# Optimization experiments

Hardware: AMD Instinct MI355X
Metric: run time of the kernel (lower is better)

## Reference

```python
import jax, jax.numpy as jnp
import numpy as np

N_ATOMS = 50000
N_EDGES = 1600000
N_ATOM_BASIS = 128
N_FILTERS = 128
N_BASIS = 25
CUTOFF = 5.0

def swish(x):
    return x * jax.nn.sigmoid(x)

def setup_inputs() -> dict:
    key = jax.random.key(0)
    ks = jax.random.split(key, 12)
    feat = jax.random.normal(ks[0], (N_ATOMS, N_ATOM_BASIS), dtype=jnp.float32)
    fij = jax.random.uniform(ks[1], (N_EDGES, N_BASIS), dtype=jnp.float32)  # RBF features in [0,1)
    rij = jax.random.uniform(ks[2], (N_EDGES,), dtype=jnp.float32) * CUTOFF  # distances in [0, cutoff)
    src = jax.random.randint(ks[3], (N_EDGES,), 0, N_ATOMS, dtype=jnp.int64)
    dst = jax.random.randint(ks[4], (N_EDGES,), 0, N_ATOMS, dtype=jnp.int64)
    s = 0.1
    W_in2f = jax.random.normal(ks[5], (N_ATOM_BASIS, N_FILTERS), dtype=jnp.float32) * s
    W_f1 = jax.random.normal(ks[6], (N_BASIS, N_FILTERS), dtype=jnp.float32) * s
    b_f1 = jax.random.normal(ks[7], (N_FILTERS,), dtype=jnp.float32) * s
    W_f2 = jax.random.normal(ks[8], (N_FILTERS, N_FILTERS), dtype=jnp.float32) * s
    b_f2 = jax.random.normal(ks[9], (N_FILTERS,), dtype=jnp.float32) * s
    W_out = jax.random.normal(ks[10], (N_FILTERS, N_ATOM_BASIS), dtype=jnp.float32) * s
    b_out = jax.random.normal(ks[11], (N_ATOM_BASIS,), dtype=jnp.float32) * s
    return {"feat": feat, "fij": fij, "rij": rij, "src": src, "dst": dst,
            "W_in2f": W_in2f, "W_f1": W_f1, "b_f1": b_f1,
            "W_f2": W_f2, "b_f2": b_f2, "W_out": W_out, "b_out": b_out}

def reference(feat, fij, rij, src, dst, W_in2f, W_f1, b_f1, W_f2, b_f2, W_out, b_out):
    # in2f: project node features to filter space (no bias, schnetpack CFConv)
    x = feat @ W_in2f                                            # [N, F]
    # filter network on RBF-expanded distances: Dense(swish) -> Dense
    Wfilt = swish(fij @ W_f1 + b_f1) @ W_f2 + b_f2               # [E, F]
    # cosine cutoff weighting
    C = 0.5 * (jnp.cos(rij * (jnp.pi / CUTOFF)) + 1.0)
    C = C * (rij < CUTOFF).astype(feat.dtype)                    # [E]
    # gather neighbor features, multiply by filter, scatter-sum to dst nodes
    m_edge = x[src] * Wfilt * C[:, None]                         # [E, F]
    agg = jax.ops.segment_sum(m_edge, dst, num_segments=N_ATOMS)  # [N, F]
    # f2out: project back to atom basis with swish activation
    return swish(agg @ W_out + b_out)                            # [N, n_atom_basis]
```

## Files before the change

### kernel.cpp

```cpp
#include <hip/hip_runtime.h>
#include <hip/hip_bf16.h>
#include <math.h>

#define N_ATOMS 50000
#define N_EDGES 1600000
#define FDIM 128
#define NB 25
#define CUTOFF_F 5.0f
#define PI_OVER_CUTOFF 0.6283185307179586f
#define NBLK 512
#define RB 196
#define P1B 782

typedef __bf16 bf16x8 __attribute__((ext_vector_type(8)));
typedef float f32x4 __attribute__((ext_vector_type(4)));

__device__ __forceinline__ float swish_f(float v) {
    return v * __builtin_amdgcn_rcpf(1.0f + __expf(-v));
}

#define SWZ(row) ((((row) & 7) ^ (((row) >> 3) & 1)) << 4)


__global__ __launch_bounds__(256) void radix1_hist_kernel(
    const int* __restrict__ dst, int* __restrict__ ebkt, int* __restrict__ gh)
{
    __shared__ int lh[RB];
    const int t = threadIdx.x;
    const int b = blockIdx.x;
    for (int i = t; i < RB; i += 256) lh[i] = 0;
    __syncthreads();
    const int base = b * 2048;
    #pragma unroll
    for (int it = 0; it < 8; ++it) {
        int i = base + it * 256 + t;
        if (i < N_EDGES) {
            int bkt = dst[i] >> 8;
            int rank = atomicAdd(&lh[bkt], 1);
            ebkt[i] = (bkt << 11) | rank;
        }
    }
    __syncthreads();
    for (int i = t; i < RB; i += 256) gh[i * P1B + b] = lh[i];
}

__global__ __launch_bounds__(256) void scan_buckets_kernel(
    const int* __restrict__ gh, int* __restrict__ off, int* __restrict__ bt)
{
    __shared__ int sa[256], sb[256];
    const int k = blockIdx.x;
    const int t = threadIdx.x;
    const int base = k * P1B;
    int v[4]; int s = 0;
    #pragma unroll
    for (int j = 0; j < 4; ++j) {
        int b = t * 4 + j;
        v[j] = (b < P1B) ? gh[base + b] : 0;
        s += v[j];
    }
    sa[t] = s;
    __syncthreads();
    int* cur = sa; int* nxt = sb;
    for (int o = 1; o < 256; o <<= 1) {
        int val = cur[t];
        if (t >= o) val += cur[t - o];
        nxt[t] = val;
        __syncthreads();
        int* tmp = cur; cur = nxt; nxt = tmp;
    }
    int run = cur[t] - s;
    #pragma unroll
    for (int j = 0; j < 4; ++j) {
        int b = t * 4 + j;
        if (b < P1B) off[base + b] = run;
        run += v[j];
    }
    if (t == 255) bt[k] = cur[t];
}

__global__ __launch_bounds__(256) void scan_base_kernel(int* __restrict__ bt) {
    __shared__ int sa[256], sb[256];
    const int t = threadIdx.x;
    int v = (t < RB) ? bt[t] : 0;
    sa[t] = v;
    __syncthreads();
    int* cur = sa; int* nxt = sb;
    for (int o = 1; o < 256; o <<= 1) {
        int val = cur[t];
        if (t >= o) val += cur[t - o];
        nxt[t] = val;
        __syncthreads();
        int* tmp = cur; cur = nxt; nxt = tmp;
    }
    if (t < RB) bt[t] = cur[t] - v;
    if (t == RB - 1) bt[RB] = cur[t];
}

__global__ __launch_bounds__(256) void radix1_place_kernel(
    const int* __restrict__ ebkt, const int* __restrict__ off,
    const int* __restrict__ bstart, int* __restrict__ ebuf1)
{
    __shared__ int obs[RB];
    const int t = threadIdx.x;
    const int b = blockIdx.x;
    if (t < RB) obs[t] = bstart[t] + off[t * P1B + b];
    __syncthreads();
    const int base = b * 2048;
    #pragma unroll
    for (int it = 0; it < 8; ++it) {
        int i = base + it * 256 + t;
        if (i < N_EDGES) {
            int p = ebkt[i];
            ebuf1[obs[p >> 11] + (p & 2047)] = i;
        }
    }
}

__global__ __launch_bounds__(1024) void radix2_kernel(
    const int* __restrict__ ebuf1, const int* __restrict__ dst,
    const int* __restrict__ bstart, int* __restrict__ perm)
{
    __shared__ int lh2[256], sa[256], sb[256], cur2[256];
    const int t = threadIdx.x;
    const int k = blockIdx.x;
    const int start = bstart[k];
    const int end = bstart[k + 1];
    if (t < 256) lh2[t] = 0;
    __syncthreads();
    for (int i = start + t; i < end; i += 1024) {
        int e = ebuf1[i];
        atomicAdd(&lh2[dst[e] & 255], 1);
    }
    __syncthreads();
    if (t < 256) sa[t] = lh2[t];
    __syncthreads();
    int* cur = sa; int* nxt = sb;
    for (int o = 1; o < 256; o <<= 1) {
        if (t < 256) {
            int val = cur[t];
            if (t >= o) val += cur[t - o];
            nxt[t] = val;
        }
        __syncthreads();
        int* tmp = cur; cur = nxt; nxt = tmp;
    }
    if (t < 256) cur2[t] = cur[t] - lh2[t];
    __syncthreads();
    for (int i = start + t; i < end; i += 1024) {
        int e = ebuf1[i];
        int r = atomicAdd(&cur2[dst[e] & 255], 1);
        perm[start + r] = e;
    }
}


__global__ void pack_b_kernel(const float* __restrict__ W, __bf16* __restrict__ out,
                              int K_eff, int KS)
{
    int idx = blockIdx.x * 256 + threadIdx.x;
    int total = KS * 8 * 64 * 8;
    if (idx >= total) return;
    int j  = idx & 7;
    int l  = (idx >> 3) & 63;
    int n  = (idx >> 9) & 7;
    int ks = idx >> 12;
    int k   = ks * 32 + ((l >> 4) << 3) + j;
    int col = (n << 4) + (l & 15);
    float v = (k < K_eff) ? W[k * FDIM + col] : 0.0f;
    out[idx] = (__bf16)v;
}


__global__ __launch_bounds__(512, 2) void node_mfma_kernel(
    const float* __restrict__ A, const __bf16* __restrict__ wp,
    const float* __restrict__ bias,
    __bf16* __restrict__ out_bf, float* __restrict__ out_f32,
    int do_swish)
{
    __shared__ __bf16 ws_[16384];

    const int t = threadIdx.x;
    const int l = t & 63;
    const int w = t >> 6;
    const int lrow = l & 15;
    const int kgrp = l >> 4;

    {
        const int4* g = (const int4*)wp;
        int4* s = (int4*)ws_;
        for (int i = t; i < 2048; i += 512) s[i] = g[i];
    }
    float br[8];
    #pragma unroll
    for (int n = 0; n < 8; ++n) br[n] = bias ? bias[(n << 4) + lrow] : 0.0f;
    __syncthreads();

    const int tile = blockIdx.x * 8 + w;
    if (tile >= N_ATOMS / 16) return;
    const int row0 = tile << 4;

    bf16x8 af[4];
    const float* ap = A + (size_t)(row0 + lrow) * FDIM + (kgrp << 3);
    #pragma unroll
    for (int ks = 0; ks < 4; ++ks) {
        float4 lo = *(const float4*)(ap + (ks << 5));
        float4 hi = *(const float4*)(ap + (ks << 5) + 4);
        af[ks][0] = (__bf16)lo.x; af[ks][1] = (__bf16)lo.y;
        af[ks][2] = (__bf16)lo.z; af[ks][3] = (__bf16)lo.w;
        af[ks][4] = (__bf16)hi.x; af[ks][5] = (__bf16)hi.y;
        af[ks][6] = (__bf16)hi.z; af[ks][7] = (__bf16)hi.w;
    }

    const f32x4 zero = {0.f, 0.f, 0.f, 0.f};
    f32x4 acc[8];
    #pragma unroll
    for (int n = 0; n < 8; ++n) acc[n] = zero;

    #pragma unroll
    for (int ks = 0; ks < 4; ++ks) {
        bf16x8 bfr[8];
        #pragma unroll
        for (int n = 0; n < 8; ++n)
            bfr[n] = *(const bf16x8*)((const char*)ws_ + (((ks << 3) + n) << 10) + (l << 4));
        #pragma unroll
        for (int n = 0; n < 8; ++n)
            acc[n] = __builtin_amdgcn_mfma_f32_16x16x32_bf16(af[ks], bfr[n], acc[n], 0, 0, 0);
    }

    if (out_bf) {
        #pragma unroll
        for (int r = 0; r < 4; ++r) {
            bf16x8 o;
            #pragma unroll
            for (int n = 0; n < 8; ++n) {
                float v = acc[n][r] + br[n];
                if (do_swish) v = swish_f(v);
                o[n] = (__bf16)v;
            }
            *(bf16x8*)&out_bf[(size_t)(row0 + (kgrp << 2) + r) * FDIM + (lrow << 3)] = o;
        }
    } else {
        #pragma unroll
        for (int r = 0; r < 4; ++r) {
            int orow = row0 + (kgrp << 2) + r;
            #pragma unroll
            for (int n = 0; n < 8; ++n) {
                float v = acc[n][r] + br[n];
                if (do_swish) v = swish_f(v);
                out_f32[(size_t)orow * FDIM + (n << 4) + lrow] = v;
            }
        }
    }
}


struct TileReg {
    float4 f0, f1;
    int   se_own, de_own;
    float rij_own;
};

__global__ __launch_bounds__(512, 2) void edge_kernel(
    const float* __restrict__ fij, const float* __restrict__ rij,
    const int* __restrict__ src, const int* __restrict__ dst,
    const int* __restrict__ perm,
    const __bf16* __restrict__ w1p, const float* __restrict__ b1,
    const __bf16* __restrict__ w2p, const float* __restrict__ b2,
    const __bf16* __restrict__ xb, float* __restrict__ agg)
{
    __shared__ __bf16 w2s[16384];
    __shared__ __bf16 hs[8][16 * 128];

    const int t = threadIdx.x;
    const int l = t & 63;
    const int w = t >> 6;
    const int lrow = l & 15;
    const int kgrp = l >> 4;

    {
        const int4* g2 = (const int4*)w2p;
        int4* s2 = (int4*)w2s;
        for (int i = t; i < 2048; i += 512) s2[i] = g2[i];
    }

    bf16x8 w1f[8];
    float b1r[8], b2r[8];
    #pragma unroll
    for (int n = 0; n < 8; ++n) {
        w1f[n] = *(const bf16x8*)(w1p + (((n << 6) + l) << 3));
        b1r[n] = b1[(n << 4) + lrow];
        b2r[n] = b2[(n << 4) + lrow];
    }
    __syncthreads();

    __bf16* hw = hs[w];
    const f32x4 zero = {0.f, 0.f, 0.f, 0.f};

    const int gw = blockIdx.x * 8 + w;
    const int NW = NBLK * 8;
    const int NT = N_EDGES / 16;
    if (gw >= NT) return;

    #define GATHER(T, pv) do { \
        const float* fp_ = fij + (size_t)(pv) * NB; \
        if (kgrp < 3) { \
            T.f0 = *(const float4*)(fp_ + (kgrp << 3)); \
            T.f1 = *(const float4*)(fp_ + (kgrp << 3) + 4); \
        } else { \
            T.f0 = make_float4(fp_[24], 0.f, 0.f, 0.f); \
            T.f1 = make_float4(0.f, 0.f, 0.f, 0.f); \
        } \
        T.se_own = src[pv]; \
        T.de_own = dst[pv]; \
        T.rij_own = rij[pv]; \
    } while (0)

    TileReg cur, nxt;
    int pvB;
    {
        int pvA = perm[((size_t)gw << 4) + lrow];
        GATHER(cur, pvA);
        int i2 = gw + NW; i2 = (i2 < NT) ? i2 : (NT - 1);
        pvB = perm[((size_t)i2 << 4) + lrow];
    }

    for (int tb = gw; tb < NT; tb += NW) {
        float Cf_own = (cur.rij_own < CUTOFF_F)
                     ? 0.5f * (__cosf(cur.rij_own * PI_OVER_CUTOFF) + 1.0f) : 0.0f;
        int se4[4], de4[4]; float Cf[4];
        #pragma unroll
        for (int r = 0; r < 4; ++r) {
            se4[r] = __shfl(cur.se_own, (kgrp << 2) + r);
            Cf[r]  = __shfl(Cf_own, (kgrp << 2) + r);
            de4[r] = __shfl(cur.de_own, (kgrp << 2) + r);
        }
        bf16x8 xv4[4];
        #pragma unroll
        for (int r = 0; r < 4; ++r)
            xv4[r] = *(const bf16x8*)&xb[(size_t)se4[r] * FDIM + (lrow << 3)];

        GATHER(nxt, pvB);
        int i3 = tb + 2 * NW; i3 = (i3 < NT) ? i3 : (NT - 1);
        pvB = perm[((size_t)i3 << 4) + lrow];

        bf16x8 a;
        a[0] = (__bf16)cur.f0.x; a[1] = (__bf16)cur.f0.y;
        a[2] = (__bf16)cur.f0.z; a[3] = (__bf16)cur.f0.w;
        a[4] = (__bf16)cur.f1.x; a[5] = (__bf16)cur.f1.y;
        a[6] = (__bf16)cur.f1.z; a[7] = (__bf16)cur.f1.w;

        #pragma unroll
        for (int n = 0; n < 8; ++n) {
            f32x4 h = __builtin_amdgcn_mfma_f32_16x16x32_bf16(a, w1f[n], zero, 0, 0, 0);
            #pragma unroll
            for (int r = 0; r < 4; ++r) {
                int hrow = (kgrp << 2) + r;
                float hv = swish_f(h[r] + b1r[n]);
                int byte = (hrow << 8) + (((n << 4) + lrow) << 1);
                byte ^= SWZ(hrow);
                *(__bf16*)((char*)hw + byte) = (__bf16)hv;
            }
        }

        f32x4 acc[8];
        #pragma unroll
        for (int n = 0; n < 8; ++n) acc[n] = zero;

        #pragma unroll
        for (int ks = 0; ks < 4; ++ks) {
            int byte = (lrow << 8) + (ks << 6) + (kgrp << 4);
            byte ^= SWZ(lrow);
            bf16x8 a2 = *(const bf16x8*)((const char*)hw + byte);
            bf16x8 bfr[8];
            #pragma unroll
            for (int n = 0; n < 8; ++n)
                bfr[n] = *(const bf16x8*)((const char*)w2s + (((ks << 3) + n) << 10) + (l << 4));
            #pragma unroll
            for (int n = 0; n < 8; ++n)
                acc[n] = __builtin_amdgcn_mfma_f32_16x16x32_bf16(a2, bfr[n], acc[n], 0, 0, 0);
        }

        int d0 = __shfl(cur.de_own, 0);
        bool uni = __all(cur.de_own == d0);

        if (uni) {
            const size_t dbase = (size_t)d0 * FDIM;
            #pragma unroll
            for (int n = 0; n < 8; ++n) {
                float s = 0.f;
                #pragma unroll
                for (int r = 0; r < 4; ++r)
                    s += (float)xv4[r][n] * (acc[n][r] + b2r[n]) * Cf[r];
                s += __shfl_xor(s, 16);
                s += __shfl_xor(s, 32);
                if (kgrp == 0) unsafeAtomicAdd(&agg[dbase + (n << 4) + lrow], s);
            }
        } else {
            const bool brk0 = (de4[0] != de4[1]);
            const bool brk1 = (de4[1] != de4[2]);
            const bool brk2 = (de4[2] != de4[3]);
            #pragma unroll
            for (int n = 0; n < 8; ++n) {
                int col = (n << 4) + lrow;
                float m[4];
                #pragma unroll
                for (int r = 0; r < 4; ++r)
                    m[r] = (float)xv4[r][n] * (acc[n][r] + b2r[n]) * Cf[r];
                float run = m[0];
                if (brk0) { unsafeAtomicAdd(&agg[(size_t)de4[0] * FDIM + col], run); run = 0.f; }
                run += m[1];
                if (brk1) { unsafeAtomicAdd(&agg[(size_t)de4[1] * FDIM + col], run); run = 0.f; }
                run += m[2];
                if (brk2) { unsafeAtomicAdd(&agg[(size_t)de4[2] * FDIM + col], run); run = 0.f; }
                run += m[3];
                unsafeAtomicAdd(&agg[(size_t)de4[3] * FDIM + col], run);
            }
        }

        cur = nxt;
    }
    #undef GATHER
}

extern "C" void kernel_launch(void* const* d_in, const int* in_sizes, int n_in,
                              void* d_out, int out_size, void* d_ws, size_t ws_size,
                              hipStream_t stream)
{
    const float* feat   = (const float*)d_in[0];
    const float* fij    = (const float*)d_in[1];
    const float* rij    = (const float*)d_in[2];
    const int*   src    = (const int*)d_in[3];
    const int*   dst    = (const int*)d_in[4];
    const float* W_in2f = (const float*)d_in[5];
    const float* W_f1   = (const float*)d_in[6];
    const float* b_f1   = (const float*)d_in[7];
    const float* W_f2   = (const float*)d_in[8];
    const float* b_f2   = (const float*)d_in[9];
    const float* W_out  = (const float*)d_in[10];
    const float* b_out  = (const float*)d_in[11];
    float* out = (float*)d_out;

    char* ws = (char*)d_ws;
    __bf16* xb    = (__bf16*)ws;
    __bf16* w1p   = (__bf16*)(ws + 12800000);
    __bf16* w2p   = (__bf16*)(ws + 12808192);
    __bf16* winp  = (__bf16*)(ws + 12840960);
    __bf16* woutp = (__bf16*)(ws + 12873728);
    int*    bt    = (int*)(ws + 12906496);
    int*    gh    = (int*)(ws + 12907520);
    int*    off   = (int*)(ws + 13520608);
    int*    ebkt  = (int*)(ws + 14133696);
    int*    ebuf1 = (int*)(ws + 20533696);
    int*    perm  = (int*)(ws + 26933696);
    float*  agg   = out;

    hipMemsetAsync(agg, 0, (size_t)N_ATOMS * FDIM * sizeof(float), stream);

    radix1_hist_kernel<<<P1B, 256, 0, stream>>>(dst, ebkt, gh);
    scan_buckets_kernel<<<RB, 256, 0, stream>>>(gh, off, bt);
    scan_base_kernel<<<1, 256, 0, stream>>>(bt);
    radix1_place_kernel<<<P1B, 256, 0, stream>>>(ebkt, off, bt, ebuf1);
    radix2_kernel<<<RB, 1024, 0, stream>>>(ebuf1, dst, bt, perm);

    pack_b_kernel<<<(4096 + 255) / 256, 256, 0, stream>>>(W_f1, w1p, NB, 1);
    pack_b_kernel<<<(16384 + 255) / 256, 256, 0, stream>>>(W_f2, w2p, 128, 4);
    pack_b_kernel<<<(16384 + 255) / 256, 256, 0, stream>>>(W_in2f, winp, 128, 4);
    pack_b_kernel<<<(16384 + 255) / 256, 256, 0, stream>>>(W_out, woutp, 128, 4);

    node_mfma_kernel<<<(N_ATOMS / 16 + 7) / 8, 512, 0, stream>>>(
        feat, winp, nullptr, xb, nullptr, 0);

    edge_kernel<<<NBLK, 512, 0, stream>>>(
        fij, rij, src, dst, perm, w1p, b_f1, w2p, b_f2, xb, agg);

    node_mfma_kernel<<<(N_ATOMS / 16 + 7) / 8, 512, 0, stream>>>(
        agg, woutp, b_out, nullptr, out, 1);
}
```

Before: 450.7 us.

## Keep filter hidden layer in registers via transposed MFMA and folded bias

The first filter-layer MFMA now runs with its operands swapped, so each lane holds a transposed output. The swished bf16 results are packed in registers to form the A operand of the second MFMA directly. For this, W_f2 rows are permuted at pack time to match the register layout, which removes the per-warp LDS staging buffer and its store/load round trip. The b_f1 bias is folded into the first GEMM as an extra K row fed by a constant 1.0 input. Blocks shrink to 256 threads with 4 blocks per CU and twice as many blocks, trading LDS for occupancy at the cost of more per-block W2 loads into shared memory.

```diff
diff --git a/kernel.cpp b/kernel.cpp
--- a/kernel.cpp
+++ b/kernel.cpp
@@ -8,7 +8,7 @@
 #define NB 25
 #define CUTOFF_F 5.0f
 #define PI_OVER_CUTOFF 0.6283185307179586f
-#define NBLK 512
+#define NBLK 1024
 #define RB 196
 #define P1B 782
 
@@ -19,7 +19,9 @@
     return v * __builtin_amdgcn_rcpf(1.0f + __expf(-v));
 }
 
-#define SWZ(row) ((((row) & 7) ^ (((row) >> 3) & 1)) << 4)
+__device__ __forceinline__ unsigned short bfbits(__bf16 x) {
+    union { __bf16 b; unsigned short u; } c; c.b = x; return c.u;
+}
 
 
 __global__ __launch_bounds__(256) void radix1_hist_kernel(
@@ -154,8 +156,8 @@
 }
 
 
-__global__ void pack_b_kernel(const float* __restrict__ W, __bf16* __restrict__ out,
-                              int K_eff, int KS)
+__global__ void pack_b_kernel(const float* __restrict__ W, const float* __restrict__ bias,
+                              __bf16* __restrict__ out, int K_eff, int KS, int perm2)
 {
     int idx = blockIdx.x * 256 + threadIdx.x;
     int total = KS * 8 * 64 * 8;
@@ -166,7 +168,12 @@
     int ks = idx >> 12;
     int k   = ks * 32 + ((l >> 4) << 3) + j;
     int col = (n << 4) + (l & 15);
-    float v = (k < K_eff) ? W[k * FDIM + col] : 0.0f;
+    int kr = k;
+    if (perm2) kr = 32 * (k >> 5) + 16 * ((k >> 2) & 1) + 4 * ((k >> 3) & 3) + (k & 3);
+    float v;
+    if (kr < K_eff) v = W[kr * FDIM + col];
+    else if (bias && kr == K_eff) v = bias[col];
+    else v = 0.0f;
     out[idx] = (__bf16)v;
 }
 
@@ -260,16 +267,15 @@
     float rij_own;
 };
 
-__global__ __launch_bounds__(512, 2) void edge_kernel(
+__global__ __launch_bounds__(256, 4) void edge_kernel(
     const float* __restrict__ fij, const float* __restrict__ rij,
     const int* __restrict__ src, const int* __restrict__ dst,
     const int* __restrict__ perm,
-    const __bf16* __restrict__ w1p, const float* __restrict__ b1,
+    const __bf16* __restrict__ w1p,
     const __bf16* __restrict__ w2p, const float* __restrict__ b2,
     const __bf16* __restrict__ xb, float* __restrict__ agg)
 {
     __shared__ __bf16 w2s[16384];
-    __shared__ __bf16 hs[8][16 * 128];
 
     const int t = threadIdx.x;
     const int l = t & 63;
@@ -280,24 +286,22 @@
     {
         const int4* g2 = (const int4*)w2p;
         int4* s2 = (int4*)w2s;
-        for (int i = t; i < 2048; i += 512) s2[i] = g2[i];
+        for (int i = t; i < 2048; i += 256) s2[i] = g2[i];
     }
 
     bf16x8 w1f[8];
-    float b1r[8], b2r[8];
+    float b2r[8];
     #pragma unroll
     for (int n = 0; n < 8; ++n) {
         w1f[n] = *(const bf16x8*)(w1p + (((n << 6) + l) << 3));
-        b1r[n] = b1[(n << 4) + lrow];
         b2r[n] = b2[(n << 4) + lrow];
     }
     __syncthreads();
 
-    __bf16* hw = hs[w];
     const f32x4 zero = {0.f, 0.f, 0.f, 0.f};
 
-    const int gw = blockIdx.x * 8 + w;
-    const int NW = NBLK * 8;
+    const int gw = blockIdx.x * 4 + w;
+    const int NW = NBLK * 4;
     const int NT = N_EDGES / 16;
     if (gw >= NT) return;
 
@@ -307,7 +311,7 @@
             T.f0 = *(const float4*)(fp_ + (kgrp << 3)); \
             T.f1 = *(const float4*)(fp_ + (kgrp << 3) + 4); \
         } else { \
-            T.f0 = make_float4(fp_[24], 0.f, 0.f, 0.f); \
+            T.f0 = make_float4(fp_[24], 1.0f, 0.f, 0.f); \
             T.f1 = make_float4(0.f, 0.f, 0.f, 0.f); \
         } \
         T.se_own = src[pv]; \
@@ -349,17 +353,16 @@
         a[4] = (__bf16)cur.f1.x; a[5] = (__bf16)cur.f1.y;
         a[6] = (__bf16)cur.f1.z; a[7] = (__bf16)cur.f1.w;
 
+        unsigned pk0[8], pk1[8];
         #pragma unroll
         for (int n = 0; n < 8; ++n) {
-            f32x4 h = __builtin_amdgcn_mfma_f32_16x16x32_bf16(a, w1f[n], zero, 0, 0, 0);
-            #pragma unroll
-            for (int r = 0; r < 4; ++r) {
-                int hrow = (kgrp << 2) + r;
-                float hv = swish_f(h[r] + b1r[n]);
-                int byte = (hrow << 8) + (((n << 4) + lrow) << 1);
-                byte ^= SWZ(hrow);
-                *(__bf16*)((char*)hw + byte) = (__bf16)hv;
-            }
+            f32x4 h = __builtin_amdgcn_mfma_f32_16x16x32_bf16(w1f[n], a, zero, 0, 0, 0);
+            __bf16 q0 = (__bf16)swish_f(h[0]);
+            __bf16 q1 = (__bf16)swish_f(h[1]);
+            __bf16 q2 = (__bf16)swish_f(h[2]);
+            __bf16 q3 = (__bf16)swish_f(h[3]);
+            pk0[n] = ((unsigned)bfbits(q1) << 16) | bfbits(q0);
+            pk1[n] = ((unsigned)bfbits(q3) << 16) | bfbits(q2);
         }
 
         f32x4 acc[8];
@@ -368,16 +371,18 @@
 
         #pragma unroll
         for (int ks = 0; ks < 4; ++ks) {
-            int byte = (lrow << 8) + (ks << 6) + (kgrp << 4);
-            byte ^= SWZ(lrow);
-            bf16x8 a2 = *(const bf16x8*)((const char*)hw + byte);
+            union { unsigned u[4]; bf16x8 v; } A2;
+            A2.u[0] = pk0[2 * ks];
+            A2.u[1] = pk1[2 * ks];
+            A2.u[2] = pk0[2 * ks + 1];
+            A2.u[3] = pk1[2 * ks + 1];
             bf16x8 bfr[8];
             #pragma unroll
             for (int n = 0; n < 8; ++n)
                 bfr[n] = *(const bf16x8*)((const char*)w2s + (((ks << 3) + n) << 10) + (l << 4));
             #pragma unroll
             for (int n = 0; n < 8; ++n)
-                acc[n] = __builtin_amdgcn_mfma_f32_16x16x32_bf16(a2, bfr[n], acc[n], 0, 0, 0);
+                acc[n] = __builtin_amdgcn_mfma_f32_16x16x32_bf16(A2.v, bfr[n], acc[n], 0, 0, 0);
         }
 
         int d0 = __shfl(cur.de_own, 0);
@@ -462,16 +467,16 @@
     radix1_place_kernel<<<P1B, 256, 0, stream>>>(ebkt, off, bt, ebuf1);
     radix2_kernel<<<RB, 1024, 0, stream>>>(ebuf1, dst, bt, perm);
 
-    pack_b_kernel<<<(4096 + 255) / 256, 256, 0, stream>>>(W_f1, w1p, NB, 1);
-    pack_b_kernel<<<(16384 + 255) / 256, 256, 0, stream>>>(W_f2, w2p, 128, 4);
-    pack_b_kernel<<<(16384 + 255) / 256, 256, 0, stream>>>(W_in2f, winp, 128, 4);
-    pack_b_kernel<<<(16384 + 255) / 256, 256, 0, stream>>>(W_out, woutp, 128, 4);
+    pack_b_kernel<<<(4096 + 255) / 256, 256, 0, stream>>>(W_f1, b_f1, w1p, NB, 1, 0);
+    pack_b_kernel<<<(16384 + 255) / 256, 256, 0, stream>>>(W_f2, nullptr, w2p, 128, 4, 1);
+    pack_b_kernel<<<(16384 + 255) / 256, 256, 0, stream>>>(W_in2f, nullptr, winp, 128, 4, 0);
+    pack_b_kernel<<<(16384 + 255) / 256, 256, 0, stream>>>(W_out, nullptr, woutp, 128, 4, 0);
 
     node_mfma_kernel<<<(N_ATOMS / 16 + 7) / 8, 512, 0, stream>>>(
         feat, winp, nullptr, xb, nullptr, 0);
 
-    edge_kernel<<<NBLK, 512, 0, stream>>>(
-        fij, rij, src, dst, perm, w1p, b_f1, w2p, b_f2, xb, agg);
+    edge_kernel<<<NBLK, 256, 0, stream>>>(
+        fij, rij, src, dst, perm, w1p, w2p, b_f2, xb, agg);
 
     node_mfma_kernel<<<(N_ATOMS / 16 + 7) / 8, 512, 0, stream>>>(
         agg, woutp, b_out, nullptr, out, 1);
```

New measurement: 934.4 us. 2.07x slower.

## Give each wave a contiguous tile range and carry same-destination sums across tiles

Applied to the files above, without the earlier changes.

Each wave now processes a contiguous block of 16-edge tiles in the dst-sorted order instead of striding across the whole edge list. When consecutive uniform tiles share the same destination atom, the partial row sum is kept in registers and only flushed by atomic add when the destination changes. The aim is fewer global atomics on agg. In exchange, prefetch locality changes and the work split across waves becomes coarser.

```diff
diff --git a/kernel.cpp b/kernel.cpp
--- a/kernel.cpp
+++ b/kernel.cpp
@@ -299,7 +299,10 @@
     const int gw = blockIdx.x * 8 + w;
     const int NW = NBLK * 8;
     const int NT = N_EDGES / 16;
-    if (gw >= NT) return;
+    const int TPW = (NT + NW - 1) / NW;
+    const int tb0 = gw * TPW;
+    if (tb0 >= NT) return;
+    int tb1 = tb0 + TPW; if (tb1 > NT) tb1 = NT;
 
     #define GATHER(T, pv) do { \
         const float* fp_ = fij + (size_t)(pv) * NB; \
@@ -318,13 +321,16 @@
     TileReg cur, nxt;
     int pvB;
     {
-        int pvA = perm[((size_t)gw << 4) + lrow];
+        int pvA = perm[((size_t)tb0 << 4) + lrow];
         GATHER(cur, pvA);
-        int i2 = gw + NW; i2 = (i2 < NT) ? i2 : (NT - 1);
+        int i2 = tb0 + 1; i2 = (i2 < NT) ? i2 : (NT - 1);
         pvB = perm[((size_t)i2 << 4) + lrow];
     }
 
-    for (int tb = gw; tb < NT; tb += NW) {
+    int dcar = -1;
+    float scar[8];
+
+    for (int tb = tb0; tb < tb1; ++tb) {
         float Cf_own = (cur.rij_own < CUTOFF_F)
                      ? 0.5f * (__cosf(cur.rij_own * PI_OVER_CUTOFF) + 1.0f) : 0.0f;
         int se4[4], de4[4]; float Cf[4];
@@ -340,7 +346,7 @@
             xv4[r] = *(const bf16x8*)&xb[(size_t)se4[r] * FDIM + (lrow << 3)];
 
         GATHER(nxt, pvB);
-        int i3 = tb + 2 * NW; i3 = (i3 < NT) ? i3 : (NT - 1);
+        int i3 = tb + 2; i3 = (i3 < NT) ? i3 : (NT - 1);
         pvB = perm[((size_t)i3 << 4) + lrow];
 
         bf16x8 a;
@@ -384,7 +390,7 @@
         bool uni = __all(cur.de_own == d0);
 
         if (uni) {
-            const size_t dbase = (size_t)d0 * FDIM;
+            float s8[8];
             #pragma unroll
             for (int n = 0; n < 8; ++n) {
                 float s = 0.f;
@@ -393,9 +399,30 @@
                     s += (float)xv4[r][n] * (acc[n][r] + b2r[n]) * Cf[r];
                 s += __shfl_xor(s, 16);
                 s += __shfl_xor(s, 32);
-                if (kgrp == 0) unsafeAtomicAdd(&agg[dbase + (n << 4) + lrow], s);
+                s8[n] = s;
+            }
+            if (d0 == dcar) {
+                #pragma unroll
+                for (int n = 0; n < 8; ++n) scar[n] += s8[n];
+            } else {
+                if (dcar >= 0 && kgrp == 0) {
+                    const size_t cb = (size_t)dcar * FDIM;
+                    #pragma unroll
+                    for (int n = 0; n < 8; ++n)
+                        unsafeAtomicAdd(&agg[cb + (n << 4) + lrow], scar[n]);
+                }
+                dcar = d0;
+                #pragma unroll
+                for (int n = 0; n < 8; ++n) scar[n] = s8[n];
             }
         } else {
+            if (dcar >= 0 && kgrp == 0) {
+                const size_t cb = (size_t)dcar * FDIM;
+                #pragma unroll
+                for (int n = 0; n < 8; ++n)
+                    unsafeAtomicAdd(&agg[cb + (n << 4) + lrow], scar[n]);
+            }
+            dcar = -1;
             const bool brk0 = (de4[0] != de4[1]);
             const bool brk1 = (de4[1] != de4[2]);
             const bool brk2 = (de4[2] != de4[3]);
@@ -419,6 +446,13 @@
 
         cur = nxt;
     }
+
+    if (dcar >= 0 && kgrp == 0) {
+        const size_t cb = (size_t)dcar * FDIM;
+        #pragma unroll
+        for (int n = 0; n < 8; ++n)
+            unsafeAtomicAdd(&agg[cb + (n << 4) + lrow], scar[n]);
+    }
     #undef GATHER
 }
 
```

Result: no change. 449.2 us (-0.3%).
